# Optimization experiments

Measured on AMD Instinct MI355X. Metric: run time of the kernel, lower is better.

## Reference

```python
import jax, jax.numpy as jnp
import numpy as np

DIM = 512
HEADS = 8
DIM_HEAD = 64
BLOCK_SIZE = 2048
B, N = 4, 2048
EPS = 1e-5


def setup_inputs() -> dict:
    key = jax.random.key(0)
    ks = jax.random.split(key, 8)
    hd = HEADS * DIM_HEAD
    std = 0.02
    return {
        "x": jax.random.normal(ks[0], (B, N, DIM), dtype=jnp.float32),
        "ln_w": jnp.ones((DIM,), jnp.float32),
        "ln_b": jnp.zeros((DIM,), jnp.float32),
        # linear weights stored [in, out]
        "wq": jax.random.normal(ks[1], (DIM, hd), jnp.float32) * std,
        "wk": jax.random.normal(ks[2], (DIM, hd), jnp.float32) * std,
        "wv": jax.random.normal(ks[3], (DIM, hd), jnp.float32) * std,
        "bv": jnp.zeros((hd,), jnp.float32),
        "wo": jax.random.normal(ks[4], (hd, DIM), jnp.float32) * std,
        "bo": jnp.zeros((DIM,), jnp.float32),
        "pe": jax.random.normal(ks[5], (1, BLOCK_SIZE, DIM), jnp.float32) * std,
    }


def reference(x, ln_w, ln_b, wq, wk, wv, bv, wo, bo, pe):
    # x: [b, n, dim] (channel_last=True path)
    b, n, _ = x.shape
    x_in = x
    # LayerNorm over last dim
    mu = jnp.mean(x, axis=-1, keepdims=True)
    var = jnp.var(x, axis=-1, keepdims=True)
    h = (x - mu) * jax.lax.rsqrt(var + EPS) * ln_w + ln_b
    # positional embedding
    h = h + pe[:, :n]
    # QKV projections -> [b, heads, n, dim_head]
    def split_heads(t):
        return t.reshape(b, n, HEADS, DIM_HEAD).transpose(0, 2, 1, 3)
    q = split_heads(h @ wq)
    k = split_heads(h @ wk)
    v = split_heads(h @ wv + bv)
    # attention
    scale = float(DIM_HEAD) ** -0.5
    attn = jnp.einsum('bhid,bhjd->bhij', q, k) * scale
    attn = jax.nn.softmax(attn, axis=-1)
    out = jnp.einsum('bhij,bhjd->bhid', attn, v)
    out = out.transpose(0, 2, 1, 3).reshape(b, n, HEADS * DIM_HEAD)
    out = out @ wo + bo
    return x_in + out
```

## Files before the change

### kernel.cpp

```cpp
#include <hip/hip_runtime.h>


typedef __bf16 bf16;
typedef __bf16 bf16x2 __attribute__((ext_vector_type(2)));
typedef __bf16 bf16x4 __attribute__((ext_vector_type(4)));
typedef __bf16 bf16x8 __attribute__((ext_vector_type(8)));
typedef float  f32x4  __attribute__((ext_vector_type(4)));
typedef float  f32x16 __attribute__((ext_vector_type(16)));
typedef unsigned int u32;
typedef u32 u32x4 __attribute__((ext_vector_type(4)));

#define MFMA16(a, b, c) __builtin_amdgcn_mfma_f32_16x16x32_bf16((a), (b), (c), 0, 0, 0)
#define MFMA32(a, b, c) __builtin_amdgcn_mfma_f32_32x32x16_bf16((a), (b), (c), 0, 0, 0)

#if __has_builtin(__builtin_amdgcn_exp2f)
#define EXP2(x) __builtin_amdgcn_exp2f(x)
#else
#define EXP2(x) exp2f(x)
#endif

__device__ __forceinline__ void gload16(const void* g, void* l) {
  __builtin_amdgcn_global_load_lds(
      (const __attribute__((address_space(1))) unsigned int*)g,
      (__attribute__((address_space(3))) unsigned int*)l, 16, 0, 0);
}

__device__ __forceinline__ u32 cvt_pk_bf16(float lo, float hi) {
  u32 r;
  asm("v_cvt_pk_bf16_f32 %0, %1, %2" : "=v"(r) : "v"(lo), "v"(hi));
  return r;
}
__device__ __forceinline__ void permswap(u32& a, u32& b) {
  asm volatile("v_permlane32_swap_b32 %0, %1" : "+v"(a), "+v"(b));
}

__global__ void wtrans_kernel(const float* __restrict__ wq, const float* __restrict__ wk,
                              const float* __restrict__ wv, const float* __restrict__ wo,
                              bf16* __restrict__ wqkvT, bf16* __restrict__ woT) {
  __shared__ float tile[32][33];
  int z = blockIdx.z;
  const float* src = (z == 0) ? wq : (z == 1) ? wk : (z == 2) ? wv : wo;
  bf16* dst = (z < 3) ? (wqkvT + (size_t)z * 512 * 512) : woT;
  int bx = blockIdx.x, by = blockIdx.y;
  int tx = threadIdx.x, ty = threadIdx.y;
#pragma unroll
  for (int yy = 0; yy < 4; ++yy)
    tile[ty + 8 * yy][tx] = src[(size_t)(by * 32 + ty + 8 * yy) * 512 + bx * 32 + tx];
  __syncthreads();
#pragma unroll
  for (int yy = 0; yy < 4; ++yy)
    dst[(size_t)(bx * 32 + ty + 8 * yy) * 512 + by * 32 + tx] = (bf16)tile[tx][ty + 8 * yy];
}

__global__ __launch_bounds__(256) void ln_pe_kernel(const float* __restrict__ x,
                                                    const float* __restrict__ w,
                                                    const float* __restrict__ b,
                                                    const float* __restrict__ pe,
                                                    bf16* __restrict__ h) {
  const int row = blockIdx.x * 4 + (threadIdx.x >> 6);
  const int lane = threadIdx.x & 63;
  const float4* xr = (const float4*)(x + (size_t)row * 512) + lane * 2;
  const float4 a = xr[0], c = xr[1];
  float s = a.x + a.y + a.z + a.w + c.x + c.y + c.z + c.w;
  float ss = a.x * a.x + a.y * a.y + a.z * a.z + a.w * a.w +
             c.x * c.x + c.y * c.y + c.z * c.z + c.w * c.w;
#pragma unroll
  for (int off = 1; off <= 32; off <<= 1) {
    s += __shfl_xor(s, off);
    ss += __shfl_xor(ss, off);
  }
  const float mu = s * (1.0f / 512.0f);
  const float var = ss * (1.0f / 512.0f) - mu * mu;
  const float rs = rsqrtf(var + 1e-5f);
  const float4* wr = (const float4*)w + lane * 2;
  const float4* br = (const float4*)b + lane * 2;
  const float4* pr = (const float4*)(pe + (size_t)(row & 2047) * 512) + lane * 2;
  const float4 w0 = wr[0], w1 = wr[1], b0 = br[0], b1 = br[1], p0 = pr[0], p1 = pr[1];
  bf16x8 o;
  o[0] = (bf16)((a.x - mu) * rs * w0.x + b0.x + p0.x);
  o[1] = (bf16)((a.y - mu) * rs * w0.y + b0.y + p0.y);
  o[2] = (bf16)((a.z - mu) * rs * w0.z + b0.z + p0.z);
  o[3] = (bf16)((a.w - mu) * rs * w0.w + b0.w + p0.w);
  o[4] = (bf16)((c.x - mu) * rs * w1.x + b1.x + p1.x);
  o[5] = (bf16)((c.y - mu) * rs * w1.y + b1.y + p1.y);
  o[6] = (bf16)((c.z - mu) * rs * w1.z + b1.z + p1.z);
  o[7] = (bf16)((c.w - mu) * rs * w1.w + b1.w + p1.w);
  *(bf16x8*)(h + (size_t)row * 512 + lane * 8) = o;
}

__device__ __forceinline__ void gemm_tile(const bf16* __restrict__ A,
                                          const bf16* __restrict__ Bt,
                                          f32x4 acc[4][4]) {
  __shared__ char lds[32768];
  const int tid = threadIdx.x, wave = tid >> 6, lane = tid & 63;
  const int wrow = wave >> 1, wcol = wave & 1;
  const int l15 = lane & 15, lg = lane >> 4;
  const char* Ab = (const char*)A + (size_t)blockIdx.x * 128 * 1024;
  const char* Bb = (const char*)Bt + (size_t)blockIdx.y * 128 * 1024;
  const int r0 = wave * 32 + (lane >> 2);
  const int cb = (lane & 3) * 16;
  const size_t so = (size_t)r0 * 1024 + cb;

  const f32x4 z = {0.f, 0.f, 0.f, 0.f};
#pragma unroll
  for (int mi = 0; mi < 4; ++mi)
#pragma unroll
    for (int ni = 0; ni < 4; ++ni) acc[mi][ni] = z;

  {
    char* nb = lds;
    gload16(Ab + so, nb + wave * 2048);
    gload16(Ab + so + 16 * 1024, nb + wave * 2048 + 1024);
    gload16(Bb + so, nb + 8192 + wave * 2048);
    gload16(Bb + so + 16 * 1024, nb + 8192 + wave * 2048 + 1024);
  }
  __syncthreads();

  for (int kt = 0; kt < 16; ++kt) {
    if (kt < 15) {
      char* nb = lds + ((kt + 1) & 1) * 16384;
      const char* As = Ab + so + (kt + 1) * 64;
      const char* Bs = Bb + so + (kt + 1) * 64;
      gload16(As, nb + wave * 2048);
      gload16(As + 16 * 1024, nb + wave * 2048 + 1024);
      gload16(Bs, nb + 8192 + wave * 2048);
      gload16(Bs + 16 * 1024, nb + 8192 + wave * 2048 + 1024);
    }
    char* lA = lds + (kt & 1) * 16384;
    char* lB = lA + 8192;
    bf16x8 av[4], bv[4];
#pragma unroll
    for (int mi = 0; mi < 4; ++mi)
      av[mi] = *(const bf16x8*)(lA + (wrow * 64 + mi * 16 + l15) * 64 + lg * 16);
#pragma unroll
    for (int ni = 0; ni < 4; ++ni)
      bv[ni] = *(const bf16x8*)(lB + (wcol * 64 + ni * 16 + l15) * 64 + lg * 16);
    __builtin_amdgcn_s_setprio(1);
#pragma unroll
    for (int mi = 0; mi < 4; ++mi)
#pragma unroll
      for (int ni = 0; ni < 4; ++ni)
        acc[mi][ni] = MFMA16(av[mi], bv[ni], acc[mi][ni]);
    __builtin_amdgcn_s_setprio(0);
    __syncthreads();
  }
}

__global__ __launch_bounds__(256, 3) void gemm_qkv_kernel(
    const bf16* __restrict__ h, const bf16* __restrict__ wqkvT,
    const float* __restrict__ bvec, bf16* __restrict__ qo, bf16* __restrict__ ko,
    bf16* __restrict__ vo) {
  f32x4 acc[4][4];
  gemm_tile(h, wqkvT, acc);
  const int tid = threadIdx.x, wave = tid >> 6, lane = tid & 63;
  const int wrow = wave >> 1, wcol = wave & 1;
  const int l15 = lane & 15, lg = lane >> 4;
  const int row0 = blockIdx.x * 128 + wrow * 64;
  const int col0 = blockIdx.y * 128 + wcol * 64;
#pragma unroll
  for (int mi = 0; mi < 4; ++mi) {
#pragma unroll
    for (int ni = 0; ni < 4; ++ni) {
      int c = col0 + ni * 16 + l15;
      int proj = c >> 9;
      int wc = c & 511;
      int head = wc >> 6, d = wc & 63;
      int rb = row0 + mi * 16 + lg * 4;
      int bb = rb >> 11, n = rb & 2047;
      if (proj == 2) {
        float bias = bvec[wc];
        bf16x4 pv;
#pragma unroll
        for (int reg = 0; reg < 4; ++reg) pv[reg] = (bf16)(acc[mi][ni][reg] + bias);
        *(bf16x4*)(vo + ((size_t)(bb * 8 + head) * 64 + d) * 2048 + n) = pv;
      } else if (proj == 0) {
#pragma unroll
        for (int reg = 0; reg < 4; ++reg)
          qo[((size_t)(bb * 8 + head) * 2048 + (n + reg)) * 64 + d] =
              (bf16)(acc[mi][ni][reg] * (0.125f * 1.44269504f));
      } else {
#pragma unroll
        for (int reg = 0; reg < 4; ++reg)
          ko[((size_t)(bb * 8 + head) * 2048 + (n + reg)) * 64 + d] =
              (bf16)acc[mi][ni][reg];
      }
    }
  }
}

__global__ __launch_bounds__(256, 2) void attn_kernel(const bf16* __restrict__ q,
                                                      const bf16* __restrict__ k,
                                                      const bf16* __restrict__ v,
                                                      bf16* __restrict__ ao) {
  __shared__ char lds[65536];
  const int tid = threadIdx.x, wave = tid >> 6, lane = tid & 63;
  const int l31 = lane & 31, hi = lane >> 5;

  const int bid = blockIdx.x;
  const int xcd = bid & 7, slot = bid >> 3;
  const int bh = xcd + 8 * (slot >> 4);
  const int qt = slot & 15;
  const int bb = bh >> 3, hh = bh & 7;

  const char* ksrc = (const char*)(k + (size_t)bh * 2048 * 64);
  const char* vsrc = (const char*)(v + (size_t)bh * 64 * 2048);

  const int krow0 = wave * 32 + (lane >> 3);
  const int kcolb = (lane & 7) * 16;
  const int vrow0 = wave * 16 + (lane >> 4);
  const int vcolb = (lane & 15) * 16;

  const int q0 = qt * 128 + wave * 32;
  const bf16* qbase = q + ((size_t)bh * 2048 + q0) * 64;
  bf16x8 qf[4];
#pragma unroll
  for (int ks = 0; ks < 4; ++ks)
    qf[ks] = *(const bf16x8*)(qbase + l31 * 64 + ks * 16 + hi * 8);

  f32x16 oacc[2] = {};
  float mrun = -1e30f, lrun = 0.f;

#define STAGE(T, BUF)                                                          \
  {                                                                            \
    char* Kd = (BUF);                                                          \
    char* Vd = (BUF) + 16384;                                                  \
    const char* kg = ksrc + (size_t)(T) * 16384;                               \
    const char* vg = vsrc + (size_t)(T) * 256;                                 \
    _Pragma("unroll") for (int i = 0; i < 4; ++i) {                            \
      int r = krow0 + i * 8;                                                   \
      gload16(kg + (size_t)r * 128 + (kcolb ^ ((r & 7) << 4)),                 \
              Kd + (wave * 32 + i * 8) * 128);                                 \
      int rv = vrow0 + i * 4;                                                  \
      gload16(vg + (size_t)rv * 4096 + (vcolb ^ ((rv & 15) << 4)),             \
              Vd + (wave * 16 + i * 4) * 256);                                 \
    }                                                                          \
  }

  STAGE(0, lds);
  __syncthreads();

  for (int t = 0; t < 16; ++t) {
    if (t + 1 < 16) STAGE(t + 1, lds + ((t + 1) & 1) * 32768);
    char* Ksh = lds + (t & 1) * 32768;
    char* Vsh = Ksh + 16384;

#pragma unroll
    for (int sub = 0; sub < 2; ++sub) {
      f32x16 sacc[2] = {};
      __builtin_amdgcn_s_setprio(1);
#pragma unroll
      for (int kt = 0; kt < 2; ++kt) {
        const int row = sub * 64 + kt * 32 + l31;
        const int swz = (row & 7) << 4;
#pragma unroll
        for (int ks = 0; ks < 4; ++ks) {
          bf16x8 kf = *(const bf16x8*)(Ksh + row * 128 + ((ks * 32 + hi * 16) ^ swz));
          sacc[kt] = MFMA32(kf, qf[ks], sacc[kt]);
        }
      }
      __builtin_amdgcn_s_setprio(0);

      float mt = sacc[0][0];
#pragma unroll
      for (int kt = 0; kt < 2; ++kt)
#pragma unroll
        for (int reg = 0; reg < 16; ++reg) mt = fmaxf(mt, sacc[kt][reg]);
      mt = fmaxf(mt, __shfl_xor(mt, 32));
      if (__any(mt > mrun + 11.5f)) {
        float mn = fmaxf(mrun, mt);
        float sc = EXP2(mrun - mn);
        mrun = mn;
        lrun *= sc;
#pragma unroll
        for (int reg = 0; reg < 16; ++reg) {
          float s2 = __shfl(sc, (reg & 3) + 8 * (reg >> 2) + 4 * hi);
          oacc[0][reg] *= s2;
          oacc[1][reg] *= s2;
        }
      }
      float rs = 0.f;
      u32 c[2][8];
#pragma unroll
      for (int kt = 0; kt < 2; ++kt)
#pragma unroll
        for (int gp = 0; gp < 4; ++gp) {
          float p0 = EXP2(sacc[kt][gp * 4 + 0] - mrun);
          float p1 = EXP2(sacc[kt][gp * 4 + 1] - mrun);
          float p2 = EXP2(sacc[kt][gp * 4 + 2] - mrun);
          float p3 = EXP2(sacc[kt][gp * 4 + 3] - mrun);
          rs += (p0 + p1) + (p2 + p3);
          c[kt][gp * 2 + 0] = cvt_pk_bf16(p0, p1);
          c[kt][gp * 2 + 1] = cvt_pk_bf16(p2, p3);
        }
      lrun += rs;

      bf16x8 pf[4];
#pragma unroll
      for (int kt = 0; kt < 2; ++kt)
#pragma unroll
        for (int mm = 0; mm < 2; ++mm) {
          u32 a0 = c[kt][mm * 4 + 0], b0 = c[kt][mm * 4 + 2];
          u32 a1 = c[kt][mm * 4 + 1], b1 = c[kt][mm * 4 + 3];
          permswap(a0, b0);
          permswap(a1, b1);
          union { u32x4 w; bf16x8 v; } u;
          u.w = (u32x4){a0, a1, b0, b1};
          pf[kt * 2 + mm] = u.v;
        }

      __builtin_amdgcn_s_setprio(1);
#pragma unroll
      for (int dt = 0; dt < 2; ++dt) {
        const int row = dt * 32 + l31;
        const int swz = (row & 15) << 4;
#pragma unroll
        for (int m = 0; m < 4; ++m) {
          bf16x8 vf = *(const bf16x8*)(Vsh + row * 256 +
                                       ((sub * 128 + m * 32 + hi * 16) ^ swz));
          oacc[dt] = MFMA32(pf[m], vf, oacc[dt]);
        }
      }
      __builtin_amdgcn_s_setprio(0);
    }
    __syncthreads();
  }
#undef STAGE

  lrun += __shfl_xor(lrun, 32);
#if __has_builtin(__builtin_amdgcn_rcpf)
  float rin = __builtin_amdgcn_rcpf(lrun);
#else
  float rin = 1.0f / lrun;
#endif
#pragma unroll
  for (int reg = 0; reg < 16; ++reg) {
    int qrow = (reg & 3) + 8 * (reg >> 2) + 4 * hi;
    float rr = __shfl(rin, qrow);
    size_t base = ((size_t)bb * 2048 + q0 + qrow) * 512 + hh * 64;
    ao[base + l31] = (bf16)(oacc[0][reg] * rr);
    ao[base + 32 + l31] = (bf16)(oacc[1][reg] * rr);
  }
}

__global__ __launch_bounds__(256, 3) void gemm_out_kernel(
    const bf16* __restrict__ ao, const bf16* __restrict__ woT,
    const float* __restrict__ bo, const float* __restrict__ x,
    float* __restrict__ out) {
  f32x4 acc[4][4];
  gemm_tile(ao, woT, acc);
  const int tid = threadIdx.x, wave = tid >> 6, lane = tid & 63;
  const int wrow = wave >> 1, wcol = wave & 1;
  const int l15 = lane & 15, lg = lane >> 4;
  const int row0 = blockIdx.x * 128 + wrow * 64;
  const int col0 = blockIdx.y * 128 + wcol * 64;
#pragma unroll
  for (int mi = 0; mi < 4; ++mi) {
#pragma unroll
    for (int ni = 0; ni < 4; ++ni) {
      int c = col0 + ni * 16 + l15;
      float bias = bo[c];
#pragma unroll
      for (int reg = 0; reg < 4; ++reg) {
        int r = row0 + mi * 16 + lg * 4 + reg;
        size_t ofs = (size_t)r * 512 + c;
        out[ofs] = acc[mi][ni][reg] + bias + x[ofs];
      }
    }
  }
}

extern "C" void kernel_launch(void* const* d_in, const int* in_sizes, int n_in,
                              void* d_out, int out_size, void* d_ws, size_t ws_size,
                              hipStream_t stream) {
  const float* x   = (const float*)d_in[0];
  const float* lnw = (const float*)d_in[1];
  const float* lnb = (const float*)d_in[2];
  const float* wq  = (const float*)d_in[3];
  const float* wk  = (const float*)d_in[4];
  const float* wv  = (const float*)d_in[5];
  const float* bv  = (const float*)d_in[6];
  const float* wo  = (const float*)d_in[7];
  const float* bo  = (const float*)d_in[8];
  const float* pe  = (const float*)d_in[9];
  float* out = (float*)d_out;

  char* ws = (char*)d_ws;
  bf16* hbuf  = (bf16*)(ws);
  bf16* wqkvT = (bf16*)(ws + 8388608);
  bf16* woT   = (bf16*)(ws + 9961472);
  bf16* qb    = (bf16*)(ws + 10485760);
  bf16* kb    = (bf16*)(ws + 18874368);
  bf16* vb    = (bf16*)(ws + 27262976);
  bf16* aob   = hbuf;

  hipLaunchKernelGGL(wtrans_kernel, dim3(16, 16, 4), dim3(32, 8), 0, stream,
                     wq, wk, wv, wo, wqkvT, woT);
  hipLaunchKernelGGL(ln_pe_kernel, dim3(2048), dim3(256), 0, stream,
                     x, lnw, lnb, pe, hbuf);
  hipLaunchKernelGGL(gemm_qkv_kernel, dim3(64, 12), dim3(256), 0, stream,
                     hbuf, wqkvT, bv, qb, kb, vb);
  hipLaunchKernelGGL(attn_kernel, dim3(512), dim3(256), 0, stream,
                     qb, kb, vb, aob);
  hipLaunchKernelGGL(gemm_out_kernel, dim3(64, 4), dim3(256), 0, stream,
                     aob, woT, bo, x, out);
}
```

Baseline: 169.7 us.

## Fuse prep kernels, stage V epilogue via LDS, retile out-proj GEMM, drop setprio

Merges the weight transpose and LayerNorm+PE kernels into one launch to save a kernel boundary. The QKV GEMM epilogue for V now stages the tile through LDS so V^T rows go out as contiguous 16-byte stores instead of scattered bf16x4 writes. The output GEMM uses a 64-row tile, doubling the grid to 512 blocks for better CU fill. The attention kernel computes both QK sub-blocks before the softmax, and setprio hints are removed from the GEMM and attention loops. These raise register pressure in attention and add LDS in the QKV kernel.

```diff
diff --git a/kernel.cpp b/kernel.cpp
--- a/kernel.cpp
+++ b/kernel.cpp
@@ -2,7 +2,6 @@
 
 
 typedef __bf16 bf16;
-typedef __bf16 bf16x2 __attribute__((ext_vector_type(2)));
 typedef __bf16 bf16x4 __attribute__((ext_vector_type(4)));
 typedef __bf16 bf16x8 __attribute__((ext_vector_type(8)));
 typedef float  f32x4  __attribute__((ext_vector_type(4)));
@@ -34,155 +33,171 @@
   asm volatile("v_permlane32_swap_b32 %0, %1" : "+v"(a), "+v"(b));
 }
 
-__global__ void wtrans_kernel(const float* __restrict__ wq, const float* __restrict__ wk,
-                              const float* __restrict__ wv, const float* __restrict__ wo,
-                              bf16* __restrict__ wqkvT, bf16* __restrict__ woT) {
-  __shared__ float tile[32][33];
-  int z = blockIdx.z;
-  const float* src = (z == 0) ? wq : (z == 1) ? wk : (z == 2) ? wv : wo;
-  bf16* dst = (z < 3) ? (wqkvT + (size_t)z * 512 * 512) : woT;
-  int bx = blockIdx.x, by = blockIdx.y;
-  int tx = threadIdx.x, ty = threadIdx.y;
-#pragma unroll
-  for (int yy = 0; yy < 4; ++yy)
-    tile[ty + 8 * yy][tx] = src[(size_t)(by * 32 + ty + 8 * yy) * 512 + bx * 32 + tx];
-  __syncthreads();
-#pragma unroll
-  for (int yy = 0; yy < 4; ++yy)
-    dst[(size_t)(bx * 32 + ty + 8 * yy) * 512 + by * 32 + tx] = (bf16)tile[tx][ty + 8 * yy];
-}
-
-__global__ __launch_bounds__(256) void ln_pe_kernel(const float* __restrict__ x,
-                                                    const float* __restrict__ w,
-                                                    const float* __restrict__ b,
-                                                    const float* __restrict__ pe,
-                                                    bf16* __restrict__ h) {
-  const int row = blockIdx.x * 4 + (threadIdx.x >> 6);
-  const int lane = threadIdx.x & 63;
-  const float4* xr = (const float4*)(x + (size_t)row * 512) + lane * 2;
-  const float4 a = xr[0], c = xr[1];
-  float s = a.x + a.y + a.z + a.w + c.x + c.y + c.z + c.w;
-  float ss = a.x * a.x + a.y * a.y + a.z * a.z + a.w * a.w +
-             c.x * c.x + c.y * c.y + c.z * c.z + c.w * c.w;
-#pragma unroll
-  for (int off = 1; off <= 32; off <<= 1) {
-    s += __shfl_xor(s, off);
-    ss += __shfl_xor(ss, off);
-  }
-  const float mu = s * (1.0f / 512.0f);
-  const float var = ss * (1.0f / 512.0f) - mu * mu;
-  const float rs = rsqrtf(var + 1e-5f);
-  const float4* wr = (const float4*)w + lane * 2;
-  const float4* br = (const float4*)b + lane * 2;
-  const float4* pr = (const float4*)(pe + (size_t)(row & 2047) * 512) + lane * 2;
-  const float4 w0 = wr[0], w1 = wr[1], b0 = br[0], b1 = br[1], p0 = pr[0], p1 = pr[1];
-  bf16x8 o;
-  o[0] = (bf16)((a.x - mu) * rs * w0.x + b0.x + p0.x);
-  o[1] = (bf16)((a.y - mu) * rs * w0.y + b0.y + p0.y);
-  o[2] = (bf16)((a.z - mu) * rs * w0.z + b0.z + p0.z);
-  o[3] = (bf16)((a.w - mu) * rs * w0.w + b0.w + p0.w);
-  o[4] = (bf16)((c.x - mu) * rs * w1.x + b1.x + p1.x);
-  o[5] = (bf16)((c.y - mu) * rs * w1.y + b1.y + p1.y);
-  o[6] = (bf16)((c.z - mu) * rs * w1.z + b1.z + p1.z);
-  o[7] = (bf16)((c.w - mu) * rs * w1.w + b1.w + p1.w);
-  *(bf16x8*)(h + (size_t)row * 512 + lane * 8) = o;
-}
-
+__global__ __launch_bounds__(256) void prep_kernel(
+    const float* __restrict__ x, const float* __restrict__ lnw,
+    const float* __restrict__ lnb, const float* __restrict__ pe,
+    const float* __restrict__ wq, const float* __restrict__ wk,
+    const float* __restrict__ wv, const float* __restrict__ wo,
+    bf16* __restrict__ h, bf16* __restrict__ wqkvT, bf16* __restrict__ woT) {
+  const int bid = blockIdx.x;
+  if (bid < 1024) {
+    __shared__ float tile[32][33];
+    const int z = bid >> 8, r = bid & 255, bx = r >> 4, by = r & 15;
+    const float* src = (z == 0) ? wq : (z == 1) ? wk : (z == 2) ? wv : wo;
+    bf16* dst = (z < 3) ? (wqkvT + (size_t)z * 262144) : woT;
+    const int tx = threadIdx.x & 31, ty = threadIdx.x >> 5;
+#pragma unroll
+    for (int yy = 0; yy < 4; ++yy)
+      tile[ty + 8 * yy][tx] = src[(size_t)(by * 32 + ty + 8 * yy) * 512 + bx * 32 + tx];
+    __syncthreads();
+#pragma unroll
+    for (int yy = 0; yy < 4; ++yy)
+      dst[(size_t)(bx * 32 + ty + 8 * yy) * 512 + by * 32 + tx] =
+          (bf16)tile[tx][ty + 8 * yy];
+  } else {
+    const int row = (bid - 1024) * 4 + (threadIdx.x >> 6);
+    const int lane = threadIdx.x & 63;
+    const float4* xr = (const float4*)(x + (size_t)row * 512) + lane * 2;
+    const float4 a = xr[0], c = xr[1];
+    float s = a.x + a.y + a.z + a.w + c.x + c.y + c.z + c.w;
+    float ss = a.x * a.x + a.y * a.y + a.z * a.z + a.w * a.w +
+               c.x * c.x + c.y * c.y + c.z * c.z + c.w * c.w;
+#pragma unroll
+    for (int off = 1; off <= 32; off <<= 1) {
+      s += __shfl_xor(s, off);
+      ss += __shfl_xor(ss, off);
+    }
+    const float mu = s * (1.0f / 512.0f);
+    const float var = ss * (1.0f / 512.0f) - mu * mu;
+    const float rs = rsqrtf(var + 1e-5f);
+    const float4* wr = (const float4*)lnw + lane * 2;
+    const float4* br = (const float4*)lnb + lane * 2;
+    const float4* pr = (const float4*)(pe + (size_t)(row & 2047) * 512) + lane * 2;
+    const float4 w0 = wr[0], w1 = wr[1], b0 = br[0], b1 = br[1], p0 = pr[0],
+                 p1 = pr[1];
+    bf16x8 o;
+    o[0] = (bf16)((a.x - mu) * rs * w0.x + b0.x + p0.x);
+    o[1] = (bf16)((a.y - mu) * rs * w0.y + b0.y + p0.y);
+    o[2] = (bf16)((a.z - mu) * rs * w0.z + b0.z + p0.z);
+    o[3] = (bf16)((a.w - mu) * rs * w0.w + b0.w + p0.w);
+    o[4] = (bf16)((c.x - mu) * rs * w1.x + b1.x + p1.x);
+    o[5] = (bf16)((c.y - mu) * rs * w1.y + b1.y + p1.y);
+    o[6] = (bf16)((c.z - mu) * rs * w1.z + b1.z + p1.z);
+    o[7] = (bf16)((c.w - mu) * rs * w1.w + b1.w + p1.w);
+    *(bf16x8*)(h + (size_t)row * 512 + lane * 8) = o;
+  }
+}
+
+template <int MI>
 __device__ __forceinline__ void gemm_tile(const bf16* __restrict__ A,
                                           const bf16* __restrict__ Bt,
-                                          f32x4 acc[4][4]) {
-  __shared__ char lds[32768];
+                                          f32x4 (&acc)[MI][4], char* lds) {
+  constexpr int BM = MI * 32;
+  constexpr int ABYTES = BM * 64;
+  constexpr int BUFB = ABYTES + 8192;
   const int tid = threadIdx.x, wave = tid >> 6, lane = tid & 63;
   const int wrow = wave >> 1, wcol = wave & 1;
   const int l15 = lane & 15, lg = lane >> 4;
-  const char* Ab = (const char*)A + (size_t)blockIdx.x * 128 * 1024;
+  const char* Ab = (const char*)A + (size_t)blockIdx.x * BM * 1024;
   const char* Bb = (const char*)Bt + (size_t)blockIdx.y * 128 * 1024;
-  const int r0 = wave * 32 + (lane >> 2);
+  const int rA = wave * (BM / 4) + (lane >> 2);
+  const int rB = wave * 32 + (lane >> 2);
   const int cb = (lane & 3) * 16;
-  const size_t so = (size_t)r0 * 1024 + cb;
 
   const f32x4 z = {0.f, 0.f, 0.f, 0.f};
 #pragma unroll
-  for (int mi = 0; mi < 4; ++mi)
+  for (int mi = 0; mi < MI; ++mi)
 #pragma unroll
     for (int ni = 0; ni < 4; ++ni) acc[mi][ni] = z;
 
-  {
-    char* nb = lds;
-    gload16(Ab + so, nb + wave * 2048);
-    gload16(Ab + so + 16 * 1024, nb + wave * 2048 + 1024);
-    gload16(Bb + so, nb + 8192 + wave * 2048);
-    gload16(Bb + so + 16 * 1024, nb + 8192 + wave * 2048 + 1024);
-  }
+#define GSTAGE(KT, NB)                                                         \
+  {                                                                            \
+    _Pragma("unroll") for (int i = 0; i < BM / 64; ++i)                        \
+        gload16(Ab + (size_t)(rA + i * 16) * 1024 + cb + (KT)*64,              \
+                (NB) + wave * (BM / 4) * 64 + i * 1024);                       \
+    _Pragma("unroll") for (int i = 0; i < 2; ++i)                              \
+        gload16(Bb + (size_t)(rB + i * 16) * 1024 + cb + (KT)*64,              \
+                (NB) + ABYTES + wave * 2048 + i * 1024);                       \
+  }
+
+  GSTAGE(0, lds);
   __syncthreads();
 
   for (int kt = 0; kt < 16; ++kt) {
-    if (kt < 15) {
-      char* nb = lds + ((kt + 1) & 1) * 16384;
-      const char* As = Ab + so + (kt + 1) * 64;
-      const char* Bs = Bb + so + (kt + 1) * 64;
-      gload16(As, nb + wave * 2048);
-      gload16(As + 16 * 1024, nb + wave * 2048 + 1024);
-      gload16(Bs, nb + 8192 + wave * 2048);
-      gload16(Bs + 16 * 1024, nb + 8192 + wave * 2048 + 1024);
-    }
-    char* lA = lds + (kt & 1) * 16384;
-    char* lB = lA + 8192;
-    bf16x8 av[4], bv[4];
-#pragma unroll
-    for (int mi = 0; mi < 4; ++mi)
-      av[mi] = *(const bf16x8*)(lA + (wrow * 64 + mi * 16 + l15) * 64 + lg * 16);
+    if (kt < 15) GSTAGE(kt + 1, lds + ((kt + 1) & 1) * BUFB);
+    char* lA = lds + (kt & 1) * BUFB;
+    char* lB = lA + ABYTES;
+    bf16x8 av[MI], bv[4];
+#pragma unroll
+    for (int mi = 0; mi < MI; ++mi)
+      av[mi] = *(const bf16x8*)(lA + (wrow * (BM / 2) + mi * 16 + l15) * 64 + lg * 16);
 #pragma unroll
     for (int ni = 0; ni < 4; ++ni)
       bv[ni] = *(const bf16x8*)(lB + (wcol * 64 + ni * 16 + l15) * 64 + lg * 16);
-    __builtin_amdgcn_s_setprio(1);
-#pragma unroll
-    for (int mi = 0; mi < 4; ++mi)
+#pragma unroll
+    for (int mi = 0; mi < MI; ++mi)
 #pragma unroll
       for (int ni = 0; ni < 4; ++ni)
         acc[mi][ni] = MFMA16(av[mi], bv[ni], acc[mi][ni]);
-    __builtin_amdgcn_s_setprio(0);
     __syncthreads();
   }
+#undef GSTAGE
 }
 
 __global__ __launch_bounds__(256, 3) void gemm_qkv_kernel(
     const bf16* __restrict__ h, const bf16* __restrict__ wqkvT,
     const float* __restrict__ bvec, bf16* __restrict__ qo, bf16* __restrict__ ko,
     bf16* __restrict__ vo) {
+  __shared__ char lds[36864];
   f32x4 acc[4][4];
-  gemm_tile(h, wqkvT, acc);
+  gemm_tile<4>(h, wqkvT, acc, lds);
   const int tid = threadIdx.x, wave = tid >> 6, lane = tid & 63;
   const int wrow = wave >> 1, wcol = wave & 1;
   const int l15 = lane & 15, lg = lane >> 4;
   const int row0 = blockIdx.x * 128 + wrow * 64;
   const int col0 = blockIdx.y * 128 + wcol * 64;
-#pragma unroll
-  for (int mi = 0; mi < 4; ++mi) {
+  if (col0 >= 1024) {
+    char* wl = lds + wave * 9216;
+    const int hh = (col0 & 511) >> 6;
 #pragma unroll
     for (int ni = 0; ni < 4; ++ni) {
-      int c = col0 + ni * 16 + l15;
-      int proj = c >> 9;
-      int wc = c & 511;
-      int head = wc >> 6, d = wc & 63;
-      int rb = row0 + mi * 16 + lg * 4;
-      int bb = rb >> 11, n = rb & 2047;
-      if (proj == 2) {
-        float bias = bvec[wc];
+      const float bias = bvec[(col0 & 511) + ni * 16 + l15];
+      const int dl = ni * 16 + l15;
+#pragma unroll
+      for (int mi = 0; mi < 4; ++mi) {
         bf16x4 pv;
 #pragma unroll
         for (int reg = 0; reg < 4; ++reg) pv[reg] = (bf16)(acc[mi][ni][reg] + bias);
-        *(bf16x4*)(vo + ((size_t)(bb * 8 + head) * 64 + d) * 2048 + n) = pv;
-      } else if (proj == 0) {
-#pragma unroll
-        for (int reg = 0; reg < 4; ++reg)
-          qo[((size_t)(bb * 8 + head) * 2048 + (n + reg)) * 64 + d] =
-              (bf16)(acc[mi][ni][reg] * (0.125f * 1.44269504f));
-      } else {
-#pragma unroll
-        for (int reg = 0; reg < 4; ++reg)
-          ko[((size_t)(bb * 8 + head) * 2048 + (n + reg)) * 64 + d] =
-              (bf16)acc[mi][ni][reg];
+        *(bf16x4*)(wl + dl * 144 + (mi * 16 + lg * 4) * 2) = pv;
+      }
+    }
+    const int bb = row0 >> 11, n0 = row0 & 2047;
+    bf16* vdst = vo + ((size_t)(bb * 8 + hh) * 64 + lane) * 2048 + n0;
+#pragma unroll
+    for (int i = 0; i < 8; ++i)
+      *((uint4*)vdst + i) = *(uint4*)(wl + lane * 144 + i * 16);
+  } else {
+#pragma unroll
+    for (int mi = 0; mi < 4; ++mi) {
+#pragma unroll
+      for (int ni = 0; ni < 4; ++ni) {
+        int c = col0 + ni * 16 + l15;
+        int proj = c >> 9;
+        int wc = c & 511;
+        int head = wc >> 6, d = wc & 63;
+        int rb = row0 + mi * 16 + lg * 4;
+        int bb = rb >> 11, n = rb & 2047;
+        if (proj == 0) {
+#pragma unroll
+          for (int reg = 0; reg < 4; ++reg)
+            qo[((size_t)(bb * 8 + head) * 2048 + (n + reg)) * 64 + d] =
+                (bf16)(acc[mi][ni][reg] * (0.125f * 1.44269504f));
+        } else {
+#pragma unroll
+          for (int reg = 0; reg < 4; ++reg)
+            ko[((size_t)(bb * 8 + head) * 2048 + (n + reg)) * 64 + d] =
+                (bf16)acc[mi][ni][reg];
+        }
       }
     }
   }
@@ -244,27 +259,30 @@
     char* Ksh = lds + (t & 1) * 32768;
     char* Vsh = Ksh + 16384;
 
+    f32x16 sacc[2][2];
 #pragma unroll
     for (int sub = 0; sub < 2; ++sub) {
-      f32x16 sacc[2] = {};
-      __builtin_amdgcn_s_setprio(1);
 #pragma unroll
       for (int kt = 0; kt < 2; ++kt) {
+        f32x16 sz = {};
         const int row = sub * 64 + kt * 32 + l31;
         const int swz = (row & 7) << 4;
 #pragma unroll
         for (int ks = 0; ks < 4; ++ks) {
           bf16x8 kf = *(const bf16x8*)(Ksh + row * 128 + ((ks * 32 + hi * 16) ^ swz));
-          sacc[kt] = MFMA32(kf, qf[ks], sacc[kt]);
-        }
-      }
-      __builtin_amdgcn_s_setprio(0);
-
-      float mt = sacc[0][0];
+          sz = MFMA32(kf, qf[ks], sz);
+        }
+        sacc[sub][kt] = sz;
+      }
+    }
+
+#pragma unroll
+    for (int sub = 0; sub < 2; ++sub) {
+      float mt = sacc[sub][0][0];
 #pragma unroll
       for (int kt = 0; kt < 2; ++kt)
 #pragma unroll
-        for (int reg = 0; reg < 16; ++reg) mt = fmaxf(mt, sacc[kt][reg]);
+        for (int reg = 0; reg < 16; ++reg) mt = fmaxf(mt, sacc[sub][kt][reg]);
       mt = fmaxf(mt, __shfl_xor(mt, 32));
       if (__any(mt > mrun + 11.5f)) {
         float mn = fmaxf(mrun, mt);
@@ -284,10 +302,10 @@
       for (int kt = 0; kt < 2; ++kt)
 #pragma unroll
         for (int gp = 0; gp < 4; ++gp) {
-          float p0 = EXP2(sacc[kt][gp * 4 + 0] - mrun);
-          float p1 = EXP2(sacc[kt][gp * 4 + 1] - mrun);
-          float p2 = EXP2(sacc[kt][gp * 4 + 2] - mrun);
-          float p3 = EXP2(sacc[kt][gp * 4 + 3] - mrun);
+          float p0 = EXP2(sacc[sub][kt][gp * 4 + 0] - mrun);
+          float p1 = EXP2(sacc[sub][kt][gp * 4 + 1] - mrun);
+          float p2 = EXP2(sacc[sub][kt][gp * 4 + 2] - mrun);
+          float p3 = EXP2(sacc[sub][kt][gp * 4 + 3] - mrun);
           rs += (p0 + p1) + (p2 + p3);
           c[kt][gp * 2 + 0] = cvt_pk_bf16(p0, p1);
           c[kt][gp * 2 + 1] = cvt_pk_bf16(p2, p3);
@@ -308,7 +326,6 @@
           pf[kt * 2 + mm] = u.v;
         }
 
-      __builtin_amdgcn_s_setprio(1);
 #pragma unroll
       for (int dt = 0; dt < 2; ++dt) {
         const int row = dt * 32 + l31;
@@ -320,7 +337,6 @@
           oacc[dt] = MFMA32(pf[m], vf, oacc[dt]);
         }
       }
-      __builtin_amdgcn_s_setprio(0);
     }
     __syncthreads();
   }
@@ -346,15 +362,16 @@
     const bf16* __restrict__ ao, const bf16* __restrict__ woT,
     const float* __restrict__ bo, const float* __restrict__ x,
     float* __restrict__ out) {
-  f32x4 acc[4][4];
-  gemm_tile(ao, woT, acc);
+  __shared__ char lds[24576];
+  f32x4 acc[2][4];
+  gemm_tile<2>(ao, woT, acc, lds);
   const int tid = threadIdx.x, wave = tid >> 6, lane = tid & 63;
   const int wrow = wave >> 1, wcol = wave & 1;
   const int l15 = lane & 15, lg = lane >> 4;
-  const int row0 = blockIdx.x * 128 + wrow * 64;
+  const int row0 = blockIdx.x * 64 + wrow * 32;
   const int col0 = blockIdx.y * 128 + wcol * 64;
 #pragma unroll
-  for (int mi = 0; mi < 4; ++mi) {
+  for (int mi = 0; mi < 2; ++mi) {
 #pragma unroll
     for (int ni = 0; ni < 4; ++ni) {
       int c = col0 + ni * 16 + l15;
@@ -393,14 +410,12 @@
   bf16* vb    = (bf16*)(ws + 27262976);
   bf16* aob   = hbuf;
 
-  hipLaunchKernelGGL(wtrans_kernel, dim3(16, 16, 4), dim3(32, 8), 0, stream,
-                     wq, wk, wv, wo, wqkvT, woT);
-  hipLaunchKernelGGL(ln_pe_kernel, dim3(2048), dim3(256), 0, stream,
-                     x, lnw, lnb, pe, hbuf);
+  hipLaunchKernelGGL(prep_kernel, dim3(3072), dim3(256), 0, stream,
+                     x, lnw, lnb, pe, wq, wk, wv, wo, hbuf, wqkvT, woT);
   hipLaunchKernelGGL(gemm_qkv_kernel, dim3(64, 12), dim3(256), 0, stream,
                      hbuf, wqkvT, bv, qb, kb, vb);
   hipLaunchKernelGGL(attn_kernel, dim3(512), dim3(256), 0, stream,
                      qb, kb, vb, aob);
-  hipLaunchKernelGGL(gemm_out_kernel, dim3(64, 4), dim3(256), 0, stream,
+  hipLaunchKernelGGL(gemm_out_kernel, dim3(128, 4), dim3(256), 0, stream,
                      aob, woT, bo, x, out);
 }
```

Result: slower. 173.7 us (+2.3%).
